# Performance work log

Hardware: AMD Instinct MI355X
Metric: run time of the kernel (lower is better)

The kernel has to match this reference:

```python
import jax, jax.numpy as jnp
import numpy as np


def setup_inputs() -> dict:
    key = jax.random.key(0)
    k1, k2 = jax.random.split(key)
    B, V = 128, 128000
    logits = jax.random.normal(k1, (B, V), dtype=jnp.float32) * 2.0
    # temperatures in [0.5, 1.5) to avoid degenerate near-zero division
    temperatures = jax.random.uniform(k2, (B,), dtype=jnp.float32, minval=0.5, maxval=1.5)
    return {"logits": logits, "temperatures": temperatures, "top_k": 50}


def reference(logits, temperatures, top_k):
    # temperature scaling (logits.float().div_(temperatures.unsqueeze(1)))
    scaled = logits.astype(jnp.float32) / temperatures[:, None]  # [B, V]
    # top-k threshold: k-th largest value per row
    kth = jax.lax.top_k(scaled, top_k)[0][:, -1, None]  # [B, 1]
    # mask everything strictly below the k-th value
    masked = jnp.where(scaled < kth, -jnp.inf, scaled)  # [B, V]
    # softmax + multinomial sample == categorical over masked logits
    # (categorical applies a stable log-softmax internally, identical distribution)
    sample_key = jax.random.key(42)
    sample_tokens = jax.random.categorical(sample_key, masked, axis=-1)  # [B] int
    return sample_tokens
```

## Files before the change

kernel.cpp:

```cpp
#include <hip/hip_runtime.h>
#include <stdint.h>

#define JAX_PARTITIONABLE 1
#define SPA   8
#define MAXC  4096
#define CPB   16

__device__ __forceinline__ void tf2x32(uint32_t c0, uint32_t c1,
                                       uint32_t& o0, uint32_t& o1) {
  const uint32_t ks0 = 0u;
  const uint32_t ks1 = 42u;
  const uint32_t ks2 = 0x1BD11BDAu ^ ks0 ^ ks1;
  uint32_t x0 = c0 + ks0;
  uint32_t x1 = c1 + ks1;
#define TF_ROUND(r) { x0 += x1; x1 = (x1 << (r)) | (x1 >> (32 - (r))); x1 ^= x0; }
  TF_ROUND(13) TF_ROUND(15) TF_ROUND(26) TF_ROUND(6)
  x0 += ks1; x1 += ks2 + 1u;
  TF_ROUND(17) TF_ROUND(29) TF_ROUND(16) TF_ROUND(24)
  x0 += ks2; x1 += ks0 + 2u;
  TF_ROUND(13) TF_ROUND(15) TF_ROUND(26) TF_ROUND(6)
  x0 += ks0; x1 += ks1 + 3u;
  TF_ROUND(17) TF_ROUND(29) TF_ROUND(16) TF_ROUND(24)
  x0 += ks1; x1 += ks2 + 4u;
  TF_ROUND(13) TF_ROUND(15) TF_ROUND(26) TF_ROUND(6)
  x0 += ks2; x1 += ks0 + 5u;
#undef TF_ROUND
  o0 = x0; o1 = x1;
}

__device__ __forceinline__ uint32_t jax_bits(uint32_t i, uint32_t half) {
#if JAX_PARTITIONABLE
  (void)half;
  uint32_t o0, o1;
  tf2x32(0u, i, o0, o1);
  return o0 ^ o1;
#else
  uint32_t o0, o1;
  if (i < half) { tf2x32(i, i + half, o0, o1); return o0; }
  else          { tf2x32(i - half, i, o0, o1); return o1; }
#endif
}

__device__ __forceinline__ float gumbel_from_bits(uint32_t b) {
  float f = __uint_as_float((b >> 9) | 0x3F800000u) - 1.0f;
  float u = f + 1.17549435e-38f;
  return -logf(-logf(u));
}

__device__ __forceinline__ uint32_t f2key(uint32_t bits) {
  return (bits & 0x80000000u) ? ~bits : (bits | 0x80000000u);
}

__global__ void zero_kernel(uint32_t* __restrict__ p, int n) {
  int i = blockIdx.x * blockDim.x + threadIdx.x;
  const int stride = gridDim.x * blockDim.x;
  for (; i < n; i += stride) p[i] = 0u;
}

__global__ __launch_bounds__(256) void hist_kernel(
    const float* __restrict__ logits, uint32_t* __restrict__ ghist, int V) {
  const int row = blockIdx.y, slice = blockIdx.x;
  const float* lrow = logits + (size_t)row * V;
  const float4* l4p = (const float4*)lrow;
  const int n4tot = V >> 2;
  const int s4 = slice * n4tot / SPA;
  const int e4 = (slice + 1) * n4tot / SPA;

  __shared__ uint32_t lh[4096];
  for (int i = threadIdx.x; i < 4096; i += 256) lh[i] = 0;
  __syncthreads();

  for (int i = s4 + threadIdx.x; i < e4; i += 256) {
    float4 l4 = l4p[i];
    float lv[4] = {l4.x, l4.y, l4.z, l4.w};
#pragma unroll
    for (int j = 0; j < 4; ++j)
      atomicAdd(&lh[f2key(__float_as_uint(lv[j])) >> 20], 1u);
  }
  if (slice == 0) {
    for (int v = (n4tot << 2) + threadIdx.x; v < V; v += 256)
      atomicAdd(&lh[f2key(__float_as_uint(lrow[v])) >> 20], 1u);
  }
  __syncthreads();

  uint32_t* gh = ghist + (size_t)row * 4096;
  for (int b = threadIdx.x; b < 4096; b += 256)
    if (lh[b]) atomicAdd(&gh[b], lh[b]);
}

__global__ __launch_bounds__(256) void selbin_kernel(
    const uint32_t* __restrict__ ghist, const int* __restrict__ topk_p,
    uint32_t* __restrict__ bin12, uint32_t* __restrict__ remk) {
  const int row = blockIdx.x;
  const uint32_t* gh = ghist + (size_t)row * 4096;
  __shared__ uint32_t lh[4096];
  __shared__ uint32_t gsum[64];
  for (int i = threadIdx.x; i < 4096; i += 256) lh[i] = gh[i];
  __syncthreads();
  if (threadIdx.x < 64) {
    uint32_t g = 0;
    for (int j = 0; j < 64; ++j) g += lh[threadIdx.x * 64 + j];
    gsum[threadIdx.x] = g;
  }
  __syncthreads();
  if (threadIdx.x == 0) {
    const uint32_t kk = (uint32_t)(*topk_p);
    uint32_t cum = 0; int g = 63;
    while (g > 0 && cum + gsum[g] < kk) { cum += gsum[g]; --g; }
    int b = g * 64 + 63;
    while (b > g * 64 && cum + lh[b] < kk) { cum += lh[b]; --b; }
    bin12[row] = (uint32_t)b;
    remk[row] = kk - cum;
  }
}

__global__ __launch_bounds__(256) void compact_kernel(
    const float* __restrict__ logits, const uint32_t* __restrict__ bin12,
    uint32_t* __restrict__ candcnt, uint32_t* __restrict__ cand, int V) {
  const int row = blockIdx.y, slice = blockIdx.x;
  const uint32_t b12 = bin12[row];
  const float* lrow = logits + (size_t)row * V;
  const float4* l4p = (const float4*)lrow;
  const int n4tot = V >> 2;
  const int s4 = slice * n4tot / SPA;
  const int e4 = (slice + 1) * n4tot / SPA;

  for (int i = s4 + threadIdx.x; i < e4; i += 256) {
    float4 l4 = l4p[i];
    float lv[4] = {l4.x, l4.y, l4.z, l4.w};
#pragma unroll
    for (int j = 0; j < 4; ++j) {
      uint32_t key = f2key(__float_as_uint(lv[j]));
      if ((key >> 20) == b12) {
        uint32_t p = atomicAdd(&candcnt[row], 1u);
        if (p < MAXC) cand[(size_t)row * MAXC + p] = key;
      }
    }
  }
  if (slice == 0) {
    for (int v = (n4tot << 2) + threadIdx.x; v < V; v += 256) {
      uint32_t key = f2key(__float_as_uint(lrow[v]));
      if ((key >> 20) == b12) {
        uint32_t p = atomicAdd(&candcnt[row], 1u);
        if (p < MAXC) cand[(size_t)row * MAXC + p] = key;
      }
    }
  }
}

__global__ __launch_bounds__(256) void selfin_kernel(
    const uint32_t* __restrict__ cand, const uint32_t* __restrict__ candcnt,
    const uint32_t* __restrict__ bin12, const uint32_t* __restrict__ remk,
    const float* __restrict__ temps, float* __restrict__ thr,
    float* __restrict__ thrRaw) {
  const int row = blockIdx.x;
  const uint32_t n = min(candcnt[row], (uint32_t)MAXC);
  const uint32_t* cr = cand + (size_t)row * MAXC;
  __shared__ uint32_t lh[4096];
  __shared__ uint32_t gsum[64];
  __shared__ uint32_t s_sel, s_rem;

  for (int i = threadIdx.x; i < 4096; i += 256) lh[i] = 0;
  __syncthreads();
  for (uint32_t i = threadIdx.x; i < n; i += 256)
    atomicAdd(&lh[(cr[i] >> 8) & 0xFFFu], 1u);
  __syncthreads();
  if (threadIdx.x < 64) {
    uint32_t g = 0;
    for (int j = 0; j < 64; ++j) g += lh[threadIdx.x * 64 + j];
    gsum[threadIdx.x] = g;
  }
  __syncthreads();
  if (threadIdx.x == 0) {
    uint32_t kk = remk[row], cum = 0; int g = 63;
    while (g > 0 && cum + gsum[g] < kk) { cum += gsum[g]; --g; }
    int b = g * 64 + 63;
    while (b > g * 64 && cum + lh[b] < kk) { cum += lh[b]; --b; }
    s_sel = (uint32_t)b;
    s_rem = kk - cum;
  }
  __syncthreads();
  const uint32_t sel12 = s_sel;
  const uint32_t kk2 = s_rem;
  __syncthreads();

  for (int i = threadIdx.x; i < 256; i += 256) lh[i] = 0;
  __syncthreads();
  for (uint32_t i = threadIdx.x; i < n; i += 256) {
    uint32_t k = cr[i];
    if (((k >> 8) & 0xFFFu) == sel12) atomicAdd(&lh[k & 0xFFu], 1u);
  }
  __syncthreads();
  if (threadIdx.x == 0) {
    uint32_t cum = 0; int b = 255;
    while (b > 0 && cum + lh[b] < kk2) { cum += lh[b]; --b; }
    uint32_t key = (bin12[row] << 20) | (sel12 << 8) | (uint32_t)b;
    uint32_t fbits = (key & 0x80000000u) ? (key & 0x7FFFFFFFu) : ~key;
    float kraw = __uint_as_float(fbits);
    thrRaw[row] = kraw;
    thr[row] = kraw / temps[row];
  }
}

__global__ __launch_bounds__(256) void sample_partial_kernel(
    const float* __restrict__ logits, const float* __restrict__ temps,
    const float* __restrict__ thr, const float* __restrict__ thr_raw,
    float* __restrict__ pval, int* __restrict__ pidx, int V, uint32_t half) {
  const int row = blockIdx.y;
  const int chunk = blockIdx.x;
  const float* lrow = logits + (size_t)row * V;
  const float4* l4p = (const float4*)lrow;
  const float temp = temps[row];
  const float kth = thr[row];
  const uint32_t kthkey = f2key(__float_as_uint(thr_raw[row]));
  const uint32_t rowBase = (uint32_t)(row * V);
  const int n4tot = V >> 2;
  const int s4 = chunk * n4tot / CPB;
  const int e4 = (chunk + 1) * n4tot / CPB;

  float best = -INFINITY;
  int bestIdx = 0x7FFFFFFF;

  for (int i = s4 + threadIdx.x; i < e4; i += 256) {
    float4 l4 = l4p[i];
    float lv[4] = {l4.x, l4.y, l4.z, l4.w};
    const int v0 = i * 4;
#pragma unroll
    for (int j = 0; j < 4; ++j) {
      uint32_t key = f2key(__float_as_uint(lv[j]));
      if (key < kthkey && (kthkey - key) > 64u) continue;
      float s = lv[j] / temp;
      if (s < kth) continue;
      uint32_t gi = rowBase + (uint32_t)(v0 + j);
      float g = gumbel_from_bits(jax_bits(gi, half));
      float val = s + g;
      int idx = v0 + j;
      if (val > best || (val == best && idx < bestIdx)) { best = val; bestIdx = idx; }
    }
  }
  if (chunk == 0) {
    for (int v = (n4tot << 2) + threadIdx.x; v < V; v += 256) {
      float lvv = lrow[v];
      uint32_t key = f2key(__float_as_uint(lvv));
      if (key < kthkey && (kthkey - key) > 64u) continue;
      float s = lvv / temp;
      if (s < kth) continue;
      float g = gumbel_from_bits(jax_bits(rowBase + (uint32_t)v, half));
      float val = s + g;
      if (val > best || (val == best && v < bestIdx)) { best = val; bestIdx = v; }
    }
  }

#pragma unroll
  for (int off = 32; off > 0; off >>= 1) {
    float ov = __shfl_down(best, off, 64);
    int oi = __shfl_down(bestIdx, off, 64);
    if (ov > best || (ov == best && oi < bestIdx)) { best = ov; bestIdx = oi; }
  }
  __shared__ float swv[4];
  __shared__ int swi[4];
  const int wid = threadIdx.x >> 6;
  const int lane = threadIdx.x & 63;
  if (lane == 0) { swv[wid] = best; swi[wid] = bestIdx; }
  __syncthreads();
  if (threadIdx.x == 0) {
    for (int w = 1; w < 4; ++w) {
      if (swv[w] > best || (swv[w] == best && swi[w] < bestIdx)) {
        best = swv[w]; bestIdx = swi[w];
      }
    }
    const int slot = row * CPB + chunk;
    pval[slot] = best;
    pidx[slot] = bestIdx;
  }
}

__global__ void reduce_kernel(const float* __restrict__ pval,
                              const int* __restrict__ pidx,
                              int* __restrict__ out, int B) {
  const int r = blockIdx.x * blockDim.x + threadIdx.x;
  if (r >= B) return;
  float best = -INFINITY;
  int bestIdx = 0x7FFFFFFF;
  for (int c = 0; c < CPB; ++c) {
    float v = pval[r * CPB + c];
    int i = pidx[r * CPB + c];
    if (v > best || (v == best && i < bestIdx)) { best = v; bestIdx = i; }
  }
  out[r] = bestIdx;
}

extern "C" void kernel_launch(void* const* d_in, const int* in_sizes, int n_in,
                              void* d_out, int out_size, void* d_ws, size_t ws_size,
                              hipStream_t stream) {
  const float* logits = (const float*)d_in[0];
  const float* temps  = (const float*)d_in[1];
  const int*   topk   = (const int*)d_in[2];
  const int B = in_sizes[1];
  const int V = in_sizes[0] / B;

  float*    thr     = (float*)d_ws;
  float*    thrRaw  = thr + B;
  uint32_t* bin12   = (uint32_t*)(thrRaw + B);
  uint32_t* remk    = bin12 + B;
  float*    pval    = (float*)(remk + B);
  int*      pidx    = (int*)(pval + (size_t)B * CPB);
  uint32_t* candcnt = (uint32_t*)(pidx + (size_t)B * CPB);
  uint32_t* ghist   = candcnt + B;
  uint32_t* cand    = ghist;

  const uint32_t half = (uint32_t)(((long long)B * (long long)V) / 2);
  const int nzero = B + B * 4096;

  zero_kernel<<<2048, 256, 0, stream>>>(candcnt, nzero);
  hist_kernel<<<dim3(SPA, B), 256, 0, stream>>>(logits, ghist, V);
  selbin_kernel<<<B, 256, 0, stream>>>(ghist, topk, bin12, remk);
  compact_kernel<<<dim3(SPA, B), 256, 0, stream>>>(logits, bin12, candcnt, cand, V);
  selfin_kernel<<<B, 256, 0, stream>>>(cand, candcnt, bin12, remk, temps, thr, thrRaw);
  sample_partial_kernel<<<dim3(CPB, B), 256, 0, stream>>>(logits, temps, thr, thrRaw,
                                                          pval, pidx, V, half);
  reduce_kernel<<<(B + 127) / 128, 128, 0, stream>>>(pval, pidx, (int*)d_out, B);
}
```

Before: 159.3 us.

## Compact all candidates at or above threshold bin and sample from compacted list

```diff
diff --git a/kernel.cpp b/kernel.cpp
--- a/kernel.cpp
+++ b/kernel.cpp
@@ -1,10 +1,8 @@
 #include <hip/hip_runtime.h>
 #include <stdint.h>
 
-#define JAX_PARTITIONABLE 1
 #define SPA   8
 #define MAXC  4096
-#define CPB   16
 
 __device__ __forceinline__ void tf2x32(uint32_t c0, uint32_t c1,
                                        uint32_t& o0, uint32_t& o1) {
@@ -28,17 +26,10 @@
   o0 = x0; o1 = x1;
 }
 
-__device__ __forceinline__ uint32_t jax_bits(uint32_t i, uint32_t half) {
-#if JAX_PARTITIONABLE
-  (void)half;
+__device__ __forceinline__ uint32_t jax_bits(uint32_t i) {
   uint32_t o0, o1;
   tf2x32(0u, i, o0, o1);
   return o0 ^ o1;
-#else
-  uint32_t o0, o1;
-  if (i < half) { tf2x32(i, i + half, o0, o1); return o0; }
-  else          { tf2x32(i - half, i, o0, o1); return o1; }
-#endif
 }
 
 __device__ __forceinline__ float gumbel_from_bits(uint32_t b) {
@@ -49,6 +40,10 @@
 
 __device__ __forceinline__ uint32_t f2key(uint32_t bits) {
   return (bits & 0x80000000u) ? ~bits : (bits | 0x80000000u);
+}
+__device__ __forceinline__ float key2f(uint32_t key) {
+  uint32_t fb = (key & 0x80000000u) ? (key & 0x7FFFFFFFu) : ~key;
+  return __uint_as_float(fb);
 }
 
 __global__ void zero_kernel(uint32_t* __restrict__ p, int n) {
@@ -116,110 +111,15 @@
 
 __global__ __launch_bounds__(256) void compact_kernel(
     const float* __restrict__ logits, const uint32_t* __restrict__ bin12,
-    uint32_t* __restrict__ candcnt, uint32_t* __restrict__ cand, int V) {
+    uint32_t* __restrict__ candcnt, uint2* __restrict__ cand, int V) {
   const int row = blockIdx.y, slice = blockIdx.x;
-  const uint32_t b12 = bin12[row];
+  const uint32_t t = bin12[row] << 20;
+  const uint32_t lo = (t >= 64u) ? t - 64u : 0u;
   const float* lrow = logits + (size_t)row * V;
   const float4* l4p = (const float4*)lrow;
   const int n4tot = V >> 2;
   const int s4 = slice * n4tot / SPA;
   const int e4 = (slice + 1) * n4tot / SPA;
-
-  for (int i = s4 + threadIdx.x; i < e4; i += 256) {
-    float4 l4 = l4p[i];
-    float lv[4] = {l4.x, l4.y, l4.z, l4.w};
-#pragma unroll
-    for (int j = 0; j < 4; ++j) {
-      uint32_t key = f2key(__float_as_uint(lv[j]));
-      if ((key >> 20) == b12) {
-        uint32_t p = atomicAdd(&candcnt[row], 1u);
-        if (p < MAXC) cand[(size_t)row * MAXC + p] = key;
-      }
-    }
-  }
-  if (slice == 0) {
-    for (int v = (n4tot << 2) + threadIdx.x; v < V; v += 256) {
-      uint32_t key = f2key(__float_as_uint(lrow[v]));
-      if ((key >> 20) == b12) {
-        uint32_t p = atomicAdd(&candcnt[row], 1u);
-        if (p < MAXC) cand[(size_t)row * MAXC + p] = key;
-      }
-    }
-  }
-}
-
-__global__ __launch_bounds__(256) void selfin_kernel(
-    const uint32_t* __restrict__ cand, const uint32_t* __restrict__ candcnt,
-    const uint32_t* __restrict__ bin12, const uint32_t* __restrict__ remk,
-    const float* __restrict__ temps, float* __restrict__ thr,
-    float* __restrict__ thrRaw) {
-  const int row = blockIdx.x;
-  const uint32_t n = min(candcnt[row], (uint32_t)MAXC);
-  const uint32_t* cr = cand + (size_t)row * MAXC;
-  __shared__ uint32_t lh[4096];
-  __shared__ uint32_t gsum[64];
-  __shared__ uint32_t s_sel, s_rem;
-
-  for (int i = threadIdx.x; i < 4096; i += 256) lh[i] = 0;
-  __syncthreads();
-  for (uint32_t i = threadIdx.x; i < n; i += 256)
-    atomicAdd(&lh[(cr[i] >> 8) & 0xFFFu], 1u);
-  __syncthreads();
-  if (threadIdx.x < 64) {
-    uint32_t g = 0;
-    for (int j = 0; j < 64; ++j) g += lh[threadIdx.x * 64 + j];
-    gsum[threadIdx.x] = g;
-  }
-  __syncthreads();
-  if (threadIdx.x == 0) {
-    uint32_t kk = remk[row], cum = 0; int g = 63;
-    while (g > 0 && cum + gsum[g] < kk) { cum += gsum[g]; --g; }
-    int b = g * 64 + 63;
-    while (b > g * 64 && cum + lh[b] < kk) { cum += lh[b]; --b; }
-    s_sel = (uint32_t)b;
-    s_rem = kk - cum;
-  }
-  __syncthreads();
-  const uint32_t sel12 = s_sel;
-  const uint32_t kk2 = s_rem;
-  __syncthreads();
-
-  for (int i = threadIdx.x; i < 256; i += 256) lh[i] = 0;
-  __syncthreads();
-  for (uint32_t i = threadIdx.x; i < n; i += 256) {
-    uint32_t k = cr[i];
-    if (((k >> 8) & 0xFFFu) == sel12) atomicAdd(&lh[k & 0xFFu], 1u);
-  }
-  __syncthreads();
-  if (threadIdx.x == 0) {
-    uint32_t cum = 0; int b = 255;
-    while (b > 0 && cum + lh[b] < kk2) { cum += lh[b]; --b; }
-    uint32_t key = (bin12[row] << 20) | (sel12 << 8) | (uint32_t)b;
-    uint32_t fbits = (key & 0x80000000u) ? (key & 0x7FFFFFFFu) : ~key;
-    float kraw = __uint_as_float(fbits);
-    thrRaw[row] = kraw;
-    thr[row] = kraw / temps[row];
-  }
-}
-
-__global__ __launch_bounds__(256) void sample_partial_kernel(
-    const float* __restrict__ logits, const float* __restrict__ temps,
-    const float* __restrict__ thr, const float* __restrict__ thr_raw,
-    float* __restrict__ pval, int* __restrict__ pidx, int V, uint32_t half) {
-  const int row = blockIdx.y;
-  const int chunk = blockIdx.x;
-  const float* lrow = logits + (size_t)row * V;
-  const float4* l4p = (const float4*)lrow;
-  const float temp = temps[row];
-  const float kth = thr[row];
-  const uint32_t kthkey = f2key(__float_as_uint(thr_raw[row]));
-  const uint32_t rowBase = (uint32_t)(row * V);
-  const int n4tot = V >> 2;
-  const int s4 = chunk * n4tot / CPB;
-  const int e4 = (chunk + 1) * n4tot / CPB;
-
-  float best = -INFINITY;
-  int bestIdx = 0x7FFFFFFF;
 
   for (int i = s4 + threadIdx.x; i < e4; i += 256) {
     float4 l4 = l4p[i];
@@ -228,27 +128,92 @@
 #pragma unroll
     for (int j = 0; j < 4; ++j) {
       uint32_t key = f2key(__float_as_uint(lv[j]));
-      if (key < kthkey && (kthkey - key) > 64u) continue;
-      float s = lv[j] / temp;
-      if (s < kth) continue;
-      uint32_t gi = rowBase + (uint32_t)(v0 + j);
-      float g = gumbel_from_bits(jax_bits(gi, half));
-      float val = s + g;
-      int idx = v0 + j;
-      if (val > best || (val == best && idx < bestIdx)) { best = val; bestIdx = idx; }
+      if (key >= lo) {
+        uint32_t p = atomicAdd(&candcnt[row], 1u);
+        if (p < MAXC) cand[(size_t)row * MAXC + p] = make_uint2(key, (uint32_t)(v0 + j));
+      }
     }
   }
-  if (chunk == 0) {
+  if (slice == 0) {
     for (int v = (n4tot << 2) + threadIdx.x; v < V; v += 256) {
-      float lvv = lrow[v];
-      uint32_t key = f2key(__float_as_uint(lvv));
-      if (key < kthkey && (kthkey - key) > 64u) continue;
-      float s = lvv / temp;
-      if (s < kth) continue;
-      float g = gumbel_from_bits(jax_bits(rowBase + (uint32_t)v, half));
-      float val = s + g;
-      if (val > best || (val == best && v < bestIdx)) { best = val; bestIdx = v; }
+      uint32_t key = f2key(__float_as_uint(lrow[v]));
+      if (key >= lo) {
+        uint32_t p = atomicAdd(&candcnt[row], 1u);
+        if (p < MAXC) cand[(size_t)row * MAXC + p] = make_uint2(key, (uint32_t)v);
+      }
     }
+  }
+}
+
+__global__ __launch_bounds__(256) void finalize_kernel(
+    const uint2* __restrict__ cand, const uint32_t* __restrict__ candcnt,
+    const uint32_t* __restrict__ bin12, const uint32_t* __restrict__ remk,
+    const float* __restrict__ temps, int* __restrict__ out, int V) {
+  const int row = blockIdx.x;
+  const uint32_t n = min(candcnt[row], (uint32_t)MAXC);
+  const uint2* cr = cand + (size_t)row * MAXC;
+  const uint32_t b12 = bin12[row];
+
+  __shared__ uint32_t lh[4096];
+  __shared__ uint32_t gsum[64];
+  __shared__ uint32_t s_sel, s_rem;
+  __shared__ float s_kth;
+
+  for (int i = threadIdx.x; i < 4096; i += 256) lh[i] = 0;
+  __syncthreads();
+  for (uint32_t i = threadIdx.x; i < n; i += 256) {
+    uint32_t k = cr[i].x;
+    if ((k >> 20) == b12) atomicAdd(&lh[(k >> 8) & 0xFFFu], 1u);
+  }
+  __syncthreads();
+  if (threadIdx.x < 64) {
+    uint32_t g = 0;
+    for (int j = 0; j < 64; ++j) g += lh[threadIdx.x * 64 + j];
+    gsum[threadIdx.x] = g;
+  }
+  __syncthreads();
+  if (threadIdx.x == 0) {
+    uint32_t kk = remk[row], cum = 0; int g = 63;
+    while (g > 0 && cum + gsum[g] < kk) { cum += gsum[g]; --g; }
+    int b = g * 64 + 63;
+    while (b > g * 64 && cum + lh[b] < kk) { cum += lh[b]; --b; }
+    s_sel = (uint32_t)b;
+    s_rem = kk - cum;
+  }
+  __syncthreads();
+  const uint32_t sel12 = s_sel;
+  const uint32_t kk2 = s_rem;
+  __syncthreads();
+
+  for (int i = threadIdx.x; i < 256; i += 256) lh[i] = 0;
+  __syncthreads();
+  const uint32_t pre24 = (b12 << 12) | sel12;
+  for (uint32_t i = threadIdx.x; i < n; i += 256) {
+    uint32_t k = cr[i].x;
+    if ((k >> 8) == pre24) atomicAdd(&lh[k & 0xFFu], 1u);
+  }
+  __syncthreads();
+  if (threadIdx.x == 0) {
+    uint32_t cum = 0; int b = 255;
+    while (b > 0 && cum + lh[b] < kk2) { cum += lh[b]; --b; }
+    uint32_t kthkey = (b12 << 20) | (sel12 << 8) | (uint32_t)b;
+    s_kth = key2f(kthkey) / temps[row];
+  }
+  __syncthreads();
+
+  const float temp = temps[row];
+  const float kth = s_kth;
+  const uint32_t rowBase = (uint32_t)(row * V);
+  float best = -INFINITY;
+  int bestIdx = 0x7FFFFFFF;
+  for (uint32_t i = threadIdx.x; i < n; i += 256) {
+    uint2 c = cr[i];
+    float s = key2f(c.x) / temp;
+    if (s < kth) continue;
+    float g = gumbel_from_bits(jax_bits(rowBase + c.y));
+    float val = s + g;
+    int idx = (int)c.y;
+    if (val > best || (val == best && idx < bestIdx)) { best = val; bestIdx = idx; }
   }
 
 #pragma unroll
@@ -269,25 +234,8 @@
         best = swv[w]; bestIdx = swi[w];
       }
     }
-    const int slot = row * CPB + chunk;
-    pval[slot] = best;
-    pidx[slot] = bestIdx;
-  }
-}
-
-__global__ void reduce_kernel(const float* __restrict__ pval,
-                              const int* __restrict__ pidx,
-                              int* __restrict__ out, int B) {
-  const int r = blockIdx.x * blockDim.x + threadIdx.x;
-  if (r >= B) return;
-  float best = -INFINITY;
-  int bestIdx = 0x7FFFFFFF;
-  for (int c = 0; c < CPB; ++c) {
-    float v = pval[r * CPB + c];
-    int i = pidx[r * CPB + c];
-    if (v > best || (v == best && i < bestIdx)) { best = v; bestIdx = i; }
-  }
-  out[r] = bestIdx;
+    out[row] = bestIdx;
+  }
 }
 
 extern "C" void kernel_launch(void* const* d_in, const int* in_sizes, int n_in,
@@ -299,25 +247,18 @@
   const int B = in_sizes[1];
   const int V = in_sizes[0] / B;
 
-  float*    thr     = (float*)d_ws;
-  float*    thrRaw  = thr + B;
-  uint32_t* bin12   = (uint32_t*)(thrRaw + B);
+  uint2*    cand    = (uint2*)d_ws;
+  uint32_t* bin12   = (uint32_t*)(cand + (size_t)B * MAXC);
   uint32_t* remk    = bin12 + B;
-  float*    pval    = (float*)(remk + B);
-  int*      pidx    = (int*)(pval + (size_t)B * CPB);
-  uint32_t* candcnt = (uint32_t*)(pidx + (size_t)B * CPB);
+  uint32_t* candcnt = remk + B;
   uint32_t* ghist   = candcnt + B;
-  uint32_t* cand    = ghist;
-
-  const uint32_t half = (uint32_t)(((long long)B * (long long)V) / 2);
+
   const int nzero = B + B * 4096;
 
   zero_kernel<<<2048, 256, 0, stream>>>(candcnt, nzero);
   hist_kernel<<<dim3(SPA, B), 256, 0, stream>>>(logits, ghist, V);
   selbin_kernel<<<B, 256, 0, stream>>>(ghist, topk, bin12, remk);
   compact_kernel<<<dim3(SPA, B), 256, 0, stream>>>(logits, bin12, candcnt, cand, V);
-  selfin_kernel<<<B, 256, 0, stream>>>(cand, candcnt, bin12, remk, temps, thr, thrRaw);
-  sample_partial_kernel<<<dim3(CPB, B), 256, 0, stream>>>(logits, temps, thr, thrRaw,
-                                                          pval, pidx, V, half);
-  reduce_kernel<<<(B + 127) / 128, 128, 0, stream>>>(pval, pidx, (int*)d_out, B);
-}
+  finalize_kernel<<<B, 256, 0, stream>>>(cand, candcnt, bin12, remk, temps,
+                                         (int*)d_out, V);
+}
```

Result: faster. 153.5 us (-3.6%).
